# Kernel optimization log

Hardware: AMD Instinct MI355X
Metric: run time of the kernel (lower is better)

## Reference

```python
import jax, jax.numpy as jnp
import numpy as np

N, E, D = 10000, 640000, 128
H1, H2, OUT = 256, 256, 64
EPS = 1e-5

def _layernorm(h, g, b):
    m = jnp.mean(h, axis=-1, keepdims=True)
    v = jnp.mean((h - m) ** 2, axis=-1, keepdims=True)
    return (h - m) * jax.lax.rsqrt(v + EPS) * g + b

def setup_inputs() -> dict:
    key = jax.random.key(0)
    ks = jax.random.split(key, 20)
    def lin(k, fan_in, fan_out):
        bound = 1.0 / np.sqrt(fan_in)
        kw, kb = jax.random.split(k)
        W = jax.random.uniform(kw, (fan_in, fan_out), jnp.float32, -bound, bound)
        b = jax.random.uniform(kb, (fan_out,), jnp.float32, -bound, bound)
        return W, b
    pool_w, pool_b = lin(ks[0], D, D)
    w1, b1 = lin(ks[1], D, H1)
    w2, b2 = lin(ks[2], H1, H2)
    mu_w, mu_b = lin(ks[3], H2, OUT)
    lv_w, lv_b = lin(ks[4], H2, OUT)
    return {
        "x": jax.random.normal(ks[5], (N, D), jnp.float32),
        "edge_index": jax.random.randint(ks[6], (2, E), 0, N, jnp.int32),
        "edge_strength": jax.random.uniform(ks[7], (E,), jnp.float32),
        "ewmc": jnp.float32(0.5),
        "pool_w": pool_w, "pool_b": pool_b,
        "lnp_g": jnp.ones((D,), jnp.float32), "lnp_b": jnp.zeros((D,), jnp.float32),
        "w1": w1, "b1": b1,
        "ln1_g": jnp.ones((H1,), jnp.float32), "ln1_b": jnp.zeros((H1,), jnp.float32),
        "w2": w2, "b2": b2,
        "ln2_g": jnp.ones((H2,), jnp.float32), "ln2_b": jnp.zeros((H2,), jnp.float32),
        "mu_w": mu_w, "mu_b": mu_b,
        "lv_w": lv_w, "lv_b": lv_b,
    }

def reference(x, edge_index, edge_strength, ewmc, pool_w, pool_b, lnp_g, lnp_b,
              w1, b1, ln1_g, ln1_b, w2, b2, ln2_g, ln2_b, mu_w, mu_b, lv_w, lv_b):
    src, dst = edge_index[0], edge_index[1]
    coef = jax.nn.softplus(ewmc)
    # [E, D] gather + edge scaling
    msgs = x[src] * (1.0 + coef * edge_strength[:, None])
    pooled = jax.nn.relu(_layernorm(msgs @ pool_w + pool_b, lnp_g, lnp_b))
    # segment max by dst; torch_scatter fills empty segments with 0 and pooled >= 0
    agg = jax.ops.segment_max(pooled, dst, num_segments=x.shape[0])
    agg = jnp.maximum(agg, 0.0)
    h = jax.nn.relu(_layernorm(agg @ w1 + b1, ln1_g, ln1_b))
    h = jax.nn.relu(_layernorm(h @ w2 + b2, ln2_g, ln2_b))
    mu = h @ mu_w + mu_b
    logvar = h @ lv_w + lv_b
    std = jnp.exp(0.5 * logvar)
    return (mu, std)
```

## Files before the change

kernel.cpp:

```cpp
#include <hip/hip_runtime.h>
#include <math.h>

#define D_DIM   128
#define H1_DIM  256
#define H2_DIM  256
#define OUT_DIM 64
#define LN_EPS  1e-5f
#define NSHARD  4

typedef __attribute__((ext_vector_type(8))) short bf16x8;
typedef __attribute__((ext_vector_type(4))) float f32x4;

__device__ __forceinline__ unsigned short bf16rne(float v) {
    unsigned int b = __float_as_uint(v);
    return (unsigned short)((b + 0x7FFFu + ((b >> 16) & 1u)) >> 16);
}

union BFPack { unsigned int u[4]; bf16x8 v; };

__global__ __launch_bounds__(512) void k_pool(
        const float* __restrict__ x, const float* __restrict__ pw,
        const float* __restrict__ pb,
        unsigned short* __restrict__ y, float4* __restrict__ stat4,
        const int* __restrict__ ei, int* __restrict__ cnt, int E, int epb,
        const float* __restrict__ w1, const float* __restrict__ w2,
        const float* __restrict__ muw, const float* __restrict__ lvw,
        short* __restrict__ wp1, short* __restrict__ wp2,
        short* __restrict__ wpH) {
    __shared__ __align__(16) short aPack[4 * 64 * 8];
    __shared__ unsigned short yLds[16][128];
    __shared__ float sPart[16][8][3];
    const int tid  = threadIdx.x;
    const int w    = tid >> 6;
    const int lane = tid & 63;
    const int gq   = lane >> 4;
    const int c16  = lane & 15;
    const int row0 = blockIdx.x * 16;

    bf16x8 bfrag[4];
    {
        const int col = w * 16 + c16;
        const int kbase = gq * 8;
#pragma unroll
        for (int kt = 0; kt < 4; ++kt) {
            int k0 = kt * 32 + kbase;
            BFPack t;
#pragma unroll
            for (int jj = 0; jj < 4; ++jj) {
                float a = pw[(k0 + 2 * jj) * D_DIM + col];
                float b = pw[(k0 + 2 * jj + 1) * D_DIM + col];
                t.u[jj] = (unsigned int)bf16rne(a) | ((unsigned int)bf16rne(b) << 16);
            }
            bfrag[kt] = t.v;
        }
    }
    {
        int ebeg = blockIdx.x * epb;
        int eend = ebeg + epb; if (eend > E) eend = E;
        for (int e = ebeg + tid; e < eend; e += 512)
            atomicAdd(&cnt[ei[E + e] * NSHARD + (e & (NSHARD - 1))], 1);
    }
    {
        int r  = tid >> 5;
        int k0 = (tid & 31) * 4;
        float4 v = *(const float4*)&x[(size_t)(row0 + r) * D_DIM + k0];
        int kt = k0 >> 5, sub = (k0 >> 3) & 3, j = k0 & 7;
        int lp = r | (sub << 4);
        unsigned int u0 = (unsigned int)bf16rne(v.x) | ((unsigned int)bf16rne(v.y) << 16);
        unsigned int u1 = (unsigned int)bf16rne(v.z) | ((unsigned int)bf16rne(v.w) << 16);
        *(uint2*)&aPack[kt * 512 + lp * 8 + j] = make_uint2(u0, u1);
    }
    __syncthreads();

    f32x4 A = {0.f, 0.f, 0.f, 0.f};
#pragma unroll
    for (int kt = 0; kt < 4; ++kt) {
        bf16x8 av = *(bf16x8*)&aPack[(kt * 64 + lane) * 8];
        A = __builtin_amdgcn_mfma_f32_16x16x32_bf16(av, bfrag[kt], A, 0, 0, 0);
    }

    {
        float pbf = pb[w * 16 + c16];
#pragma unroll
        for (int r = 0; r < 4; ++r) {
            unsigned short h = bf16rne(A[r]);
            yLds[gq * 4 + r][w * 16 + c16] = h;
            float hf = __uint_as_float((unsigned int)h << 16);
            float s1 = hf, s2 = hf * hf, s3 = hf * pbf;
#pragma unroll
            for (int m = 1; m < 16; m <<= 1) {
                s1 += __shfl_xor(s1, m, 64);
                s2 += __shfl_xor(s2, m, 64);
                s3 += __shfl_xor(s3, m, 64);
            }
            if (c16 == 0) {
                sPart[gq * 4 + r][w][0] = s1;
                sPart[gq * 4 + r][w][1] = s2;
                sPart[gq * 4 + r][w][2] = s3;
            }
        }
    }
    __syncthreads();
    {
        int idx = tid * 4;
        int r = idx >> 7, c = idx & 127;
        *(uint2*)&y[(size_t)(row0 + r) * D_DIM + c] = *(const uint2*)&yLds[r][c];
    }
    if (tid < 16) {
        float t1 = 0.f, t2 = 0.f, t3 = 0.f;
#pragma unroll
        for (int ww = 0; ww < 8; ++ww) {
            t1 += sPart[tid][ww][0]; t2 += sPart[tid][ww][1]; t3 += sPart[tid][ww][2];
        }
        stat4[row0 + tid] = make_float4(t1 * (1.f / 128.f), t2 * (1.f / 128.f),
                                        t3 * (1.f / 128.f), 0.f);
    }
    if (blockIdx.x < 32) {
        int i = blockIdx.x * 512 + tid;
        const float* W; int Ndim, kt, ln, col; short* dst;
        if (i < 4096) {
            int q = i >> 6; ln = i & 63; kt = q & 3; int ct = q >> 2;
            W = w1; Ndim = H1_DIM; col = ct * 16 + (ln & 15); dst = wp1 + i * 8;
        } else if (i < 12288) {
            int i2 = i - 4096; int q = i2 >> 6; ln = i2 & 63; kt = q & 7; int ct = q >> 3;
            W = w2; Ndim = H2_DIM; col = ct * 16 + (ln & 15); dst = wp2 + i2 * 8;
        } else {
            int i3 = i - 12288; int q = i3 >> 6; ln = i3 & 63; kt = q & 7; int ct = q >> 3;
            Ndim = OUT_DIM; dst = wpH + i3 * 8;
            if (ct < 4) { W = muw; col = ct * 16 + (ln & 15); }
            else        { W = lvw; col = (ct - 4) * 16 + (ln & 15); }
        }
        int k0 = kt * 32 + (ln >> 4) * 8;
        unsigned int u[4];
#pragma unroll
        for (int jj = 0; jj < 4; ++jj) {
            float a = W[(k0 + 2 * jj) * Ndim + col];
            float b = W[(k0 + 2 * jj + 1) * Ndim + col];
            u[jj] = (unsigned int)bf16rne(a) | ((unsigned int)bf16rne(b) << 16);
        }
        *(uint4*)dst = make_uint4(u[0], u[1], u[2], u[3]);
    }
}

__global__ __launch_bounds__(1024) void k_scanA(
        const int* __restrict__ cnt, int* __restrict__ offs,
        int* __restrict__ bsum, int N4) {
    __shared__ int part[1024];
    const int t = threadIdx.x;
    const int idx = blockIdx.x * 1024 + t;
    int v = (idx < N4) ? cnt[idx] : 0;
    part[t] = v;
    __syncthreads();
    for (int off = 1; off < 1024; off <<= 1) {
        int n = (t >= off) ? part[t - off] : 0;
        __syncthreads();
        part[t] += n;
        __syncthreads();
    }
    if (idx < N4) offs[idx] = part[t] - v;
    if (t == 1023) bsum[blockIdx.x] = part[t];
}

__global__ __launch_bounds__(64) void k_scanB(
        const int* __restrict__ bsum, int* __restrict__ bbase,
        int* __restrict__ offs, float* __restrict__ consts,
        const float* __restrict__ ewmc, const float* __restrict__ pb,
        int nblk, int N4) {
    const int l = threadIdx.x;
    {
        float v0 = pb[l], v1 = pb[l + 64];
        float s1 = v0 + v1, s2 = v0 * v0 + v1 * v1;
#pragma unroll
        for (int off = 1; off < 64; off <<= 1) {
            s1 += __shfl_xor(s1, off, 64);
            s2 += __shfl_xor(s2, off, 64);
        }
        if (l == 0) {
            float xw = ewmc[0];
            consts[0] = (xw > 30.f) ? xw : log1pf(expf(xw));
            consts[1] = s1 * (1.f / 128.f);
            consts[2] = s2 * (1.f / 128.f);
        }
    }
    int val = (l < nblk) ? bsum[l] : 0;
    int orig = val;
#pragma unroll
    for (int off = 1; off < 64; off <<= 1) {
        int n = __shfl_up(val, off, 64);
        if (l >= off) val += n;
    }
    if (l < nblk) bbase[l] = val - orig;
    if (l == nblk - 1) offs[N4] = val;
}

__global__ __launch_bounds__(1024) void k_scanC(
        int* __restrict__ offs, int* __restrict__ head,
        const int* __restrict__ bbase, int N4) {
    int idx = blockIdx.x * 1024 + threadIdx.x;
    if (idx < N4) {
        int o = offs[idx] + bbase[blockIdx.x];
        offs[idx] = o;
        head[idx] = o;
    }
}

__global__ __launch_bounds__(256) void k_scatter(
        const int* __restrict__ ei, const float* __restrict__ es,
        const float* __restrict__ consts, const float4* __restrict__ stat4,
        int* __restrict__ head, float4* __restrict__ pairs, int E) {
    const float coef = consts[0], mpb = consts[1], mpb2 = consts[2];
    const int tid = threadIdx.x;
    const int e0 = blockIdx.x * 1024 + tid;
    int srcv[4], dstv[4]; float sv[4]; float4 st[4]; int pos[4]; bool ok[4];
#pragma unroll
    for (int u = 0; u < 4; ++u) {
        int e = e0 + u * 256;
        ok[u] = (e < E);
        if (ok[u]) { srcv[u] = ei[e]; dstv[u] = ei[E + e]; sv[u] = es[e]; }
    }
#pragma unroll
    for (int u = 0; u < 4; ++u) if (ok[u]) st[u] = stat4[srcv[u]];
#pragma unroll
    for (int u = 0; u < 4; ++u) if (ok[u]) {
        int e = e0 + u * 256;
        pos[u] = atomicAdd(&head[dstv[u] * NSHARD + (e & (NSHARD - 1))], 1);
    }
#pragma unroll
    for (int u = 0; u < 4; ++u) if (ok[u]) {
        float s = fmaf(coef, sv[u], 1.0f);
        float m   = fmaf(s, st[u].x, mpb);
        float et2 = fmaf(s * s, st[u].y, fmaf(2.f * s, st[u].z, mpb2));
        float inv = rsqrtf(et2 - m * m + LN_EPS);
        pairs[pos[u]] = make_float4(__int_as_float(srcv[u]), s, m, inv);
    }
}

#define GPROC(P, YB)                                                          \
    {                                                                         \
        float s = (P).y, m = (P).z, inv = (P).w;                              \
        float y0 = __uint_as_float((YB).x << 16);                             \
        float y1 = __uint_as_float((YB).x & 0xFFFF0000u);                     \
        float y2 = __uint_as_float((YB).y << 16);                             \
        float y3 = __uint_as_float((YB).y & 0xFFFF0000u);                     \
        float y4 = __uint_as_float((YB).z << 16);                             \
        float y5 = __uint_as_float((YB).z & 0xFFFF0000u);                     \
        float y6 = __uint_as_float((YB).w << 16);                             \
        float y7 = __uint_as_float((YB).w & 0xFFFF0000u);                     \
        mxA.x = fmaxf(mxA.x, fmaf(fmaf(s, y0, pbA.x) - m, inv * gA.x, bA.x)); \
        mxA.y = fmaxf(mxA.y, fmaf(fmaf(s, y1, pbA.y) - m, inv * gA.y, bA.y)); \
        mxA.z = fmaxf(mxA.z, fmaf(fmaf(s, y2, pbA.z) - m, inv * gA.z, bA.z)); \
        mxA.w = fmaxf(mxA.w, fmaf(fmaf(s, y3, pbA.w) - m, inv * gA.w, bA.w)); \
        mxB.x = fmaxf(mxB.x, fmaf(fmaf(s, y4, pbB.x) - m, inv * gB.x, bB.x)); \
        mxB.y = fmaxf(mxB.y, fmaf(fmaf(s, y5, pbB.y) - m, inv * gB.y, bB.y)); \
        mxB.z = fmaxf(mxB.z, fmaf(fmaf(s, y6, pbB.z) - m, inv * gB.z, bB.z)); \
        mxB.w = fmaxf(mxB.w, fmaf(fmaf(s, y7, pbB.w) - m, inv * gB.w, bB.w)); \
    }

__global__ __launch_bounds__(256) void k_gather(
        const float4* __restrict__ pairs, const int* __restrict__ offs,
        const unsigned short* __restrict__ y, const float* __restrict__ pb,
        const float* __restrict__ g, const float* __restrict__ b,
        float* __restrict__ agg, int N) {
    const int node = blockIdx.x * 4 + (threadIdx.x >> 6);
    if (node >= N) return;
    const int lane = threadIdx.x & 63;
    const int sub  = lane >> 4;
    const int q    = lane & 15;
    const int d0   = q * 8;
    const float4 pbA = *(const float4*)&pb[d0], pbB = *(const float4*)&pb[d0 + 4];
    const float4 gA  = *(const float4*)&g[d0],  gB  = *(const float4*)&g[d0 + 4];
    const float4 bA  = *(const float4*)&b[d0],  bB  = *(const float4*)&b[d0 + 4];
    float4 mxA = make_float4(-INFINITY, -INFINITY, -INFINITY, -INFINITY);
    float4 mxB = mxA;
    int j = offs[node * NSHARD];
    const int end = offs[node * NSHARD + NSHARD];
    for (; j + 12 <= end; j += 12) {
        float4 p[3]; uint4 yb[3];
#pragma unroll
        for (int u = 0; u < 3; ++u) p[u] = pairs[j + 4 * u + sub];
#pragma unroll
        for (int u = 0; u < 3; ++u)
            yb[u] = *(const uint4*)&y[(size_t)__float_as_int(p[u].x) * D_DIM + d0];
#pragma unroll
        for (int u = 0; u < 3; ++u) GPROC(p[u], yb[u]);
    }
    for (; j + 4 <= end; j += 4) {
        float4 p = pairs[j + sub];
        uint4 yb = *(const uint4*)&y[(size_t)__float_as_int(p.x) * D_DIM + d0];
        GPROC(p, yb);
    }
    if (j < end) {
        int rem = end - j;
        float4 p = pairs[j + (sub < rem ? sub : 0)];
        uint4 yb = *(const uint4*)&y[(size_t)__float_as_int(p.x) * D_DIM + d0];
        GPROC(p, yb);
    }
    mxA.x = fmaxf(mxA.x, __shfl_xor(mxA.x, 16, 64));
    mxA.y = fmaxf(mxA.y, __shfl_xor(mxA.y, 16, 64));
    mxA.z = fmaxf(mxA.z, __shfl_xor(mxA.z, 16, 64));
    mxA.w = fmaxf(mxA.w, __shfl_xor(mxA.w, 16, 64));
    mxB.x = fmaxf(mxB.x, __shfl_xor(mxB.x, 16, 64));
    mxB.y = fmaxf(mxB.y, __shfl_xor(mxB.y, 16, 64));
    mxB.z = fmaxf(mxB.z, __shfl_xor(mxB.z, 16, 64));
    mxB.w = fmaxf(mxB.w, __shfl_xor(mxB.w, 16, 64));
    mxA.x = fmaxf(mxA.x, __shfl_xor(mxA.x, 32, 64));
    mxA.y = fmaxf(mxA.y, __shfl_xor(mxA.y, 32, 64));
    mxA.z = fmaxf(mxA.z, __shfl_xor(mxA.z, 32, 64));
    mxA.w = fmaxf(mxA.w, __shfl_xor(mxA.w, 32, 64));
    mxB.x = fmaxf(mxB.x, __shfl_xor(mxB.x, 32, 64));
    mxB.y = fmaxf(mxB.y, __shfl_xor(mxB.y, 32, 64));
    mxB.z = fmaxf(mxB.z, __shfl_xor(mxB.z, 32, 64));
    mxB.w = fmaxf(mxB.w, __shfl_xor(mxB.w, 32, 64));
    if (sub == 0) {
        float4 oA, oB;
        oA.x = fmaxf(mxA.x, 0.f); oA.y = fmaxf(mxA.y, 0.f);
        oA.z = fmaxf(mxA.z, 0.f); oA.w = fmaxf(mxA.w, 0.f);
        oB.x = fmaxf(mxB.x, 0.f); oB.y = fmaxf(mxB.y, 0.f);
        oB.z = fmaxf(mxB.z, 0.f); oB.w = fmaxf(mxB.w, 0.f);
        *(float4*)&agg[(size_t)node * D_DIM + d0]     = oA;
        *(float4*)&agg[(size_t)node * D_DIM + d0 + 4] = oB;
    }
}

__global__ __launch_bounds__(512) void k_mlp(
        const float* __restrict__ agg,
        const short* __restrict__ wp1, const short* __restrict__ wp2,
        const short* __restrict__ wpH,
        const float* __restrict__ b1, const float* __restrict__ g1,
        const float* __restrict__ bb1,
        const float* __restrict__ b2, const float* __restrict__ g2,
        const float* __restrict__ bb2,
        const float* __restrict__ mub, const float* __restrict__ lvb,
        float* __restrict__ out, int N) {
    __shared__ __align__(16) short aPack[8 * 64 * 8];
    __shared__ float sPart[16][8][2];
    __shared__ float sM[16], sI[16];
    const int tid  = threadIdx.x;
    const int w    = tid >> 6;
    const int lane = tid & 63;
    const int gq   = lane >> 4;
    const int c16  = lane & 15;
    const int row0 = blockIdx.x * 16;

    {
        int r  = tid >> 5;
        int k0 = (tid & 31) * 4;
        float4 v = *(const float4*)&agg[(size_t)(row0 + r) * D_DIM + k0];
        int kt = k0 >> 5, sub = (k0 >> 3) & 3, j = k0 & 7;
        int lp = r | (sub << 4);
        unsigned int u0 = (unsigned int)bf16rne(v.x) | ((unsigned int)bf16rne(v.y) << 16);
        unsigned int u1 = (unsigned int)bf16rne(v.z) | ((unsigned int)bf16rne(v.w) << 16);
        *(uint2*)&aPack[kt * 512 + lp * 8 + j] = make_uint2(u0, u1);
    }
    __syncthreads();

    const int ct0 = 2 * w, ct1 = 2 * w + 1;
    f32x4 A0 = {0.f, 0.f, 0.f, 0.f}, A1 = {0.f, 0.f, 0.f, 0.f};

#pragma unroll
    for (int kt = 0; kt < 4; ++kt) {
        bf16x8 av = *(bf16x8*)&aPack[(kt * 64 + lane) * 8];
        bf16x8 bv0 = *(const bf16x8*)&wp1[((ct0 * 4 + kt) * 64 + lane) * 8];
        bf16x8 bv1 = *(const bf16x8*)&wp1[((ct1 * 4 + kt) * 64 + lane) * 8];
        A0 = __builtin_amdgcn_mfma_f32_16x16x32_bf16(av, bv0, A0, 0, 0, 0);
        A1 = __builtin_amdgcn_mfma_f32_16x16x32_bf16(av, bv1, A1, 0, 0, 0);
    }
    {
        int col0 = ct0 * 16 + c16, col1 = ct1 * 16 + c16;
        float bias0 = b1[col0], bias1 = b1[col1];
        float v0[4], v1[4];
#pragma unroll
        for (int r = 0; r < 4; ++r) {
            v0[r] = A0[r] + bias0; v1[r] = A1[r] + bias1;
            float s1 = v0[r] + v1[r];
            float s2 = v0[r] * v0[r] + v1[r] * v1[r];
#pragma unroll
            for (int m = 1; m < 16; m <<= 1) {
                s1 += __shfl_xor(s1, m, 64);
                s2 += __shfl_xor(s2, m, 64);
            }
            if (c16 == 0) { sPart[gq * 4 + r][w][0] = s1; sPart[gq * 4 + r][w][1] = s2; }
        }
        __syncthreads();
        if (tid < 16) {
            float t1 = 0.f, t2 = 0.f;
#pragma unroll
            for (int ww = 0; ww < 8; ++ww) { t1 += sPart[tid][ww][0]; t2 += sPart[tid][ww][1]; }
            float m = t1 * (1.f / 256.f);
            sM[tid] = m;
            sI[tid] = rsqrtf(t2 * (1.f / 256.f) - m * m + LN_EPS);
        }
        __syncthreads();
        float gc0 = g1[col0], bc0 = bb1[col0];
        float gc1 = g1[col1], bc1 = bb1[col1];
#pragma unroll
        for (int r = 0; r < 4; ++r) {
            int row = gq * 4 + r;
            float m = sM[row], inv = sI[row];
            float h0 = fmaxf(fmaf((v0[r] - m) * inv, gc0, bc0), 0.f);
            float h1 = fmaxf(fmaf((v1[r] - m) * inv, gc1, bc1), 0.f);
            aPack[(col0 >> 5) * 512 + (row | (((col0 >> 3) & 3) << 4)) * 8 + (col0 & 7)] = (short)bf16rne(h0);
            aPack[(col1 >> 5) * 512 + (row | (((col1 >> 3) & 3) << 4)) * 8 + (col1 & 7)] = (short)bf16rne(h1);
        }
    }
    __syncthreads();

    A0 = (f32x4){0.f, 0.f, 0.f, 0.f}; A1 = (f32x4){0.f, 0.f, 0.f, 0.f};
#pragma unroll
    for (int kt = 0; kt < 8; ++kt) {
        bf16x8 av = *(bf16x8*)&aPack[(kt * 64 + lane) * 8];
        bf16x8 bv0 = *(const bf16x8*)&wp2[((ct0 * 8 + kt) * 64 + lane) * 8];
        bf16x8 bv1 = *(const bf16x8*)&wp2[((ct1 * 8 + kt) * 64 + lane) * 8];
        A0 = __builtin_amdgcn_mfma_f32_16x16x32_bf16(av, bv0, A0, 0, 0, 0);
        A1 = __builtin_amdgcn_mfma_f32_16x16x32_bf16(av, bv1, A1, 0, 0, 0);
    }
    {
        int col0 = ct0 * 16 + c16, col1 = ct1 * 16 + c16;
        float bias0 = b2[col0], bias1 = b2[col1];
        float v0[4], v1[4];
#pragma unroll
        for (int r = 0; r < 4; ++r) {
            v0[r] = A0[r] + bias0; v1[r] = A1[r] + bias1;
            float s1 = v0[r] + v1[r];
            float s2 = v0[r] * v0[r] + v1[r] * v1[r];
#pragma unroll
            for (int m = 1; m < 16; m <<= 1) {
                s1 += __shfl_xor(s1, m, 64);
                s2 += __shfl_xor(s2, m, 64);
            }
            if (c16 == 0) { sPart[gq * 4 + r][w][0] = s1; sPart[gq * 4 + r][w][1] = s2; }
        }
        __syncthreads();
        if (tid < 16) {
            float t1 = 0.f, t2 = 0.f;
#pragma unroll
            for (int ww = 0; ww < 8; ++ww) { t1 += sPart[tid][ww][0]; t2 += sPart[tid][ww][1]; }
            float m = t1 * (1.f / 256.f);
            sM[tid] = m;
            sI[tid] = rsqrtf(t2 * (1.f / 256.f) - m * m + LN_EPS);
        }
        __syncthreads();
        float gc0 = g2[col0], bc0 = bb2[col0];
        float gc1 = g2[col1], bc1 = bb2[col1];
#pragma unroll
        for (int r = 0; r < 4; ++r) {
            int row = gq * 4 + r;
            float m = sM[row], inv = sI[row];
            float h0 = fmaxf(fmaf((v0[r] - m) * inv, gc0, bc0), 0.f);
            float h1 = fmaxf(fmaf((v1[r] - m) * inv, gc1, bc1), 0.f);
            aPack[(col0 >> 5) * 512 + (row | (((col0 >> 3) & 3) << 4)) * 8 + (col0 & 7)] = (short)bf16rne(h0);
            aPack[(col1 >> 5) * 512 + (row | (((col1 >> 3) & 3) << 4)) * 8 + (col1 & 7)] = (short)bf16rne(h1);
        }
    }
    __syncthreads();

    {
        f32x4 H = {0.f, 0.f, 0.f, 0.f};
#pragma unroll
        for (int kt = 0; kt < 8; ++kt) {
            bf16x8 av = *(bf16x8*)&aPack[(kt * 64 + lane) * 8];
            bf16x8 bv = *(const bf16x8*)&wpH[((w * 8 + kt) * 64 + lane) * 8];
            H = __builtin_amdgcn_mfma_f32_16x16x32_bf16(av, bv, H, 0, 0, 0);
        }
        int colh = (w & 3) * 16 + c16;
        if (w < 4) {
            float bias = mub[colh];
#pragma unroll
            for (int r = 0; r < 4; ++r)
                out[(size_t)(row0 + gq * 4 + r) * OUT_DIM + colh] = H[r] + bias;
        } else {
            float bias = lvb[colh];
#pragma unroll
            for (int r = 0; r < 4; ++r)
                out[(size_t)N * OUT_DIM + (size_t)(row0 + gq * 4 + r) * OUT_DIM + colh] =
                    expf(0.5f * (H[r] + bias));
        }
    }
}

extern "C" void kernel_launch(void* const* d_in, const int* in_sizes, int n_in,
                              void* d_out, int out_size, void* d_ws, size_t ws_size,
                              hipStream_t stream) {
    const float* x      = (const float*)d_in[0];
    const int*   ei     = (const int*)  d_in[1];
    const float* es     = (const float*)d_in[2];
    const float* ewmc   = (const float*)d_in[3];
    const float* pool_w = (const float*)d_in[4];
    const float* pool_b = (const float*)d_in[5];
    const float* lnp_g  = (const float*)d_in[6];
    const float* lnp_b  = (const float*)d_in[7];
    const float* w1     = (const float*)d_in[8];
    const float* b1     = (const float*)d_in[9];
    const float* ln1_g  = (const float*)d_in[10];
    const float* ln1_b  = (const float*)d_in[11];
    const float* w2     = (const float*)d_in[12];
    const float* b2     = (const float*)d_in[13];
    const float* ln2_g  = (const float*)d_in[14];
    const float* ln2_b  = (const float*)d_in[15];
    const float* mu_w   = (const float*)d_in[16];
    const float* mu_b   = (const float*)d_in[17];
    const float* lv_w   = (const float*)d_in[18];
    const float* lv_b   = (const float*)d_in[19];

    const int N  = in_sizes[0] / D_DIM;
    const int E  = in_sizes[2];
    const int N4 = N * NSHARD;
    const int nblkScan = (N4 + 1023) / 1024;

    float*  ws     = (float*)d_ws;
    float*  consts = ws;
    float4* stat4  = (float4*)(ws + 16);
    unsigned short* y = (unsigned short*)(ws + 16 + 4 * (size_t)N);
    float*  agg    = ws + 16 + 4 * (size_t)N + (size_t)N * D_DIM / 2;
    size_t  w      = 16 + 4 * (size_t)N + (size_t)N * D_DIM / 2 + (size_t)N * D_DIM;
    int*    cnt    = (int*)(ws + w); w += N4;
    int*    offs   = (int*)(ws + w); w += N4 + 1;
    int*    head   = (int*)(ws + w); w += N4;
    int*    bsum   = (int*)(ws + w); w += 64;
    int*    bbase  = (int*)(ws + w); w += 64;
    w = (w + 3) & ~(size_t)3;
    short*  wp1    = (short*)(ws + w); w += 16384;
    short*  wp2    = (short*)(ws + w); w += 32768;
    short*  wpH    = (short*)(ws + w); w += 16384;
    float4* pairs  = (float4*)(ws + w);

    const int nbPool = N / 16;
    const int epb    = (E + nbPool - 1) / nbPool;

    hipMemsetAsync(cnt, 0, (size_t)N4 * sizeof(int), stream);
    k_pool<<<nbPool, 512, 0, stream>>>(x, pool_w, pool_b, y, stat4, ei, cnt, E,
                                       epb, w1, w2, mu_w, lv_w, wp1, wp2, wpH);
    k_scanA<<<nblkScan, 1024, 0, stream>>>(cnt, offs, bsum, N4);
    k_scanB<<<1, 64, 0, stream>>>(bsum, bbase, offs, consts, ewmc, pool_b,
                                  nblkScan, N4);
    k_scanC<<<nblkScan, 1024, 0, stream>>>(offs, head, bbase, N4);
    k_scatter<<<(E + 1023) / 1024, 256, 0, stream>>>(ei, es, consts, stat4,
                                                     head, pairs, E);
    k_gather<<<(N + 3) / 4, 256, 0, stream>>>(pairs, offs, y,
                                              pool_b, lnp_g, lnp_b, agg, N);
    k_mlp<<<N / 16, 512, 0, stream>>>(agg, wp1, wp2, wpH,
                                      b1, ln1_g, ln1_b,
                                      b2, ln2_g, ln2_b,
                                      mu_b, lv_b, (float*)d_out, N);
}
```

Baseline: 118.5 us.

## Fuse segment-max gather into MLP kernel and widen scatter per-thread work

Merges the gather/segment-max kernel into the MLP kernel. Each of the 8 waves in a 512-thread block aggregates two of the block's 16 nodes and writes bf16 results straight into the shared-memory A-pack, so the fp32 agg buffer is never written to or read from global memory. Separately, the scatter kernel now handles 8 edges per thread instead of 4, halving its grid size. The fusion saves a kernel launch and the agg round trip, but gives the MLP blocks a serial, load-imbalanced gather phase with fewer nodes in flight per wave, which may hide gather latency less well.

```diff
diff --git a/kernel.cpp b/kernel.cpp
--- a/kernel.cpp
+++ b/kernel.cpp
@@ -210,23 +210,23 @@
         int* __restrict__ head, float4* __restrict__ pairs, int E) {
     const float coef = consts[0], mpb = consts[1], mpb2 = consts[2];
     const int tid = threadIdx.x;
-    const int e0 = blockIdx.x * 1024 + tid;
-    int srcv[4], dstv[4]; float sv[4]; float4 st[4]; int pos[4]; bool ok[4];
-#pragma unroll
-    for (int u = 0; u < 4; ++u) {
+    const int e0 = blockIdx.x * 2048 + tid;
+    int srcv[8], dstv[8]; float sv[8]; float4 st[8]; int pos[8]; bool ok[8];
+#pragma unroll
+    for (int u = 0; u < 8; ++u) {
         int e = e0 + u * 256;
         ok[u] = (e < E);
         if (ok[u]) { srcv[u] = ei[e]; dstv[u] = ei[E + e]; sv[u] = es[e]; }
     }
 #pragma unroll
-    for (int u = 0; u < 4; ++u) if (ok[u]) st[u] = stat4[srcv[u]];
-#pragma unroll
-    for (int u = 0; u < 4; ++u) if (ok[u]) {
+    for (int u = 0; u < 8; ++u) if (ok[u]) st[u] = stat4[srcv[u]];
+#pragma unroll
+    for (int u = 0; u < 8; ++u) if (ok[u]) {
         int e = e0 + u * 256;
         pos[u] = atomicAdd(&head[dstv[u] * NSHARD + (e & (NSHARD - 1))], 1);
     }
 #pragma unroll
-    for (int u = 0; u < 4; ++u) if (ok[u]) {
+    for (int u = 0; u < 8; ++u) if (ok[u]) {
         float s = fmaf(coef, sv[u], 1.0f);
         float m   = fmaf(s, st[u].x, mpb);
         float et2 = fmaf(s * s, st[u].y, fmaf(2.f * s, st[u].z, mpb2));
@@ -256,74 +256,10 @@
         mxB.w = fmaxf(mxB.w, fmaf(fmaf(s, y7, pbB.w) - m, inv * gB.w, bB.w)); \
     }
 
-__global__ __launch_bounds__(256) void k_gather(
+__global__ __launch_bounds__(512) void k_gmlp(
         const float4* __restrict__ pairs, const int* __restrict__ offs,
         const unsigned short* __restrict__ y, const float* __restrict__ pb,
         const float* __restrict__ g, const float* __restrict__ b,
-        float* __restrict__ agg, int N) {
-    const int node = blockIdx.x * 4 + (threadIdx.x >> 6);
-    if (node >= N) return;
-    const int lane = threadIdx.x & 63;
-    const int sub  = lane >> 4;
-    const int q    = lane & 15;
-    const int d0   = q * 8;
-    const float4 pbA = *(const float4*)&pb[d0], pbB = *(const float4*)&pb[d0 + 4];
-    const float4 gA  = *(const float4*)&g[d0],  gB  = *(const float4*)&g[d0 + 4];
-    const float4 bA  = *(const float4*)&b[d0],  bB  = *(const float4*)&b[d0 + 4];
-    float4 mxA = make_float4(-INFINITY, -INFINITY, -INFINITY, -INFINITY);
-    float4 mxB = mxA;
-    int j = offs[node * NSHARD];
-    const int end = offs[node * NSHARD + NSHARD];
-    for (; j + 12 <= end; j += 12) {
-        float4 p[3]; uint4 yb[3];
-#pragma unroll
-        for (int u = 0; u < 3; ++u) p[u] = pairs[j + 4 * u + sub];
-#pragma unroll
-        for (int u = 0; u < 3; ++u)
-            yb[u] = *(const uint4*)&y[(size_t)__float_as_int(p[u].x) * D_DIM + d0];
-#pragma unroll
-        for (int u = 0; u < 3; ++u) GPROC(p[u], yb[u]);
-    }
-    for (; j + 4 <= end; j += 4) {
-        float4 p = pairs[j + sub];
-        uint4 yb = *(const uint4*)&y[(size_t)__float_as_int(p.x) * D_DIM + d0];
-        GPROC(p, yb);
-    }
-    if (j < end) {
-        int rem = end - j;
-        float4 p = pairs[j + (sub < rem ? sub : 0)];
-        uint4 yb = *(const uint4*)&y[(size_t)__float_as_int(p.x) * D_DIM + d0];
-        GPROC(p, yb);
-    }
-    mxA.x = fmaxf(mxA.x, __shfl_xor(mxA.x, 16, 64));
-    mxA.y = fmaxf(mxA.y, __shfl_xor(mxA.y, 16, 64));
-    mxA.z = fmaxf(mxA.z, __shfl_xor(mxA.z, 16, 64));
-    mxA.w = fmaxf(mxA.w, __shfl_xor(mxA.w, 16, 64));
-    mxB.x = fmaxf(mxB.x, __shfl_xor(mxB.x, 16, 64));
-    mxB.y = fmaxf(mxB.y, __shfl_xor(mxB.y, 16, 64));
-    mxB.z = fmaxf(mxB.z, __shfl_xor(mxB.z, 16, 64));
-    mxB.w = fmaxf(mxB.w, __shfl_xor(mxB.w, 16, 64));
-    mxA.x = fmaxf(mxA.x, __shfl_xor(mxA.x, 32, 64));
-    mxA.y = fmaxf(mxA.y, __shfl_xor(mxA.y, 32, 64));
-    mxA.z = fmaxf(mxA.z, __shfl_xor(mxA.z, 32, 64));
-    mxA.w = fmaxf(mxA.w, __shfl_xor(mxA.w, 32, 64));
-    mxB.x = fmaxf(mxB.x, __shfl_xor(mxB.x, 32, 64));
-    mxB.y = fmaxf(mxB.y, __shfl_xor(mxB.y, 32, 64));
-    mxB.z = fmaxf(mxB.z, __shfl_xor(mxB.z, 32, 64));
-    mxB.w = fmaxf(mxB.w, __shfl_xor(mxB.w, 32, 64));
-    if (sub == 0) {
-        float4 oA, oB;
-        oA.x = fmaxf(mxA.x, 0.f); oA.y = fmaxf(mxA.y, 0.f);
-        oA.z = fmaxf(mxA.z, 0.f); oA.w = fmaxf(mxA.w, 0.f);
-        oB.x = fmaxf(mxB.x, 0.f); oB.y = fmaxf(mxB.y, 0.f);
-        oB.z = fmaxf(mxB.z, 0.f); oB.w = fmaxf(mxB.w, 0.f);
-        *(float4*)&agg[(size_t)node * D_DIM + d0]     = oA;
-        *(float4*)&agg[(size_t)node * D_DIM + d0 + 4] = oB;
-    }
-}
-
-__global__ __launch_bounds__(512) void k_mlp(
-        const float* __restrict__ agg,
         const short* __restrict__ wp1, const short* __restrict__ wp2,
         const short* __restrict__ wpH,
         const float* __restrict__ b1, const float* __restrict__ g1,
@@ -343,14 +279,70 @@
     const int row0 = blockIdx.x * 16;
 
     {
-        int r  = tid >> 5;
-        int k0 = (tid & 31) * 4;
-        float4 v = *(const float4*)&agg[(size_t)(row0 + r) * D_DIM + k0];
-        int kt = k0 >> 5, sub = (k0 >> 3) & 3, j = k0 & 7;
-        int lp = r | (sub << 4);
-        unsigned int u0 = (unsigned int)bf16rne(v.x) | ((unsigned int)bf16rne(v.y) << 16);
-        unsigned int u1 = (unsigned int)bf16rne(v.z) | ((unsigned int)bf16rne(v.w) << 16);
-        *(uint2*)&aPack[kt * 512 + lp * 8 + j] = make_uint2(u0, u1);
+        const int sub = lane >> 4;
+        const int q   = lane & 15;
+        const int d0  = q * 8;
+        const float4 pbA = *(const float4*)&pb[d0], pbB = *(const float4*)&pb[d0 + 4];
+        const float4 gA  = *(const float4*)&g[d0],  gB  = *(const float4*)&g[d0 + 4];
+        const float4 bA  = *(const float4*)&b[d0],  bB  = *(const float4*)&b[d0 + 4];
+#pragma unroll
+        for (int nn = 0; nn < 2; ++nn) {
+            const int r = 2 * w + nn;
+            const int node = row0 + r;
+            float4 mxA = make_float4(-INFINITY, -INFINITY, -INFINITY, -INFINITY);
+            float4 mxB = mxA;
+            int j = offs[node * NSHARD];
+            const int end = offs[node * NSHARD + NSHARD];
+            for (; j + 12 <= end; j += 12) {
+                float4 p[3]; uint4 yb[3];
+#pragma unroll
+                for (int u = 0; u < 3; ++u) p[u] = pairs[j + 4 * u + sub];
+#pragma unroll
+                for (int u = 0; u < 3; ++u)
+                    yb[u] = *(const uint4*)&y[(size_t)__float_as_int(p[u].x) * D_DIM + d0];
+#pragma unroll
+                for (int u = 0; u < 3; ++u) GPROC(p[u], yb[u]);
+            }
+            for (; j + 4 <= end; j += 4) {
+                float4 p = pairs[j + sub];
+                uint4 yb = *(const uint4*)&y[(size_t)__float_as_int(p.x) * D_DIM + d0];
+                GPROC(p, yb);
+            }
+            if (j < end) {
+                int rem = end - j;
+                float4 p = pairs[j + (sub < rem ? sub : 0)];
+                uint4 yb = *(const uint4*)&y[(size_t)__float_as_int(p.x) * D_DIM + d0];
+                GPROC(p, yb);
+            }
+            mxA.x = fmaxf(mxA.x, __shfl_xor(mxA.x, 16, 64));
+            mxA.y = fmaxf(mxA.y, __shfl_xor(mxA.y, 16, 64));
+            mxA.z = fmaxf(mxA.z, __shfl_xor(mxA.z, 16, 64));
+            mxA.w = fmaxf(mxA.w, __shfl_xor(mxA.w, 16, 64));
+            mxB.x = fmaxf(mxB.x, __shfl_xor(mxB.x, 16, 64));
+            mxB.y = fmaxf(mxB.y, __shfl_xor(mxB.y, 16, 64));
+            mxB.z = fmaxf(mxB.z, __shfl_xor(mxB.z, 16, 64));
+            mxB.w = fmaxf(mxB.w, __shfl_xor(mxB.w, 16, 64));
+            mxA.x = fmaxf(mxA.x, __shfl_xor(mxA.x, 32, 64));
+            mxA.y = fmaxf(mxA.y, __shfl_xor(mxA.y, 32, 64));
+            mxA.z = fmaxf(mxA.z, __shfl_xor(mxA.z, 32, 64));
+            mxA.w = fmaxf(mxA.w, __shfl_xor(mxA.w, 32, 64));
+            mxB.x = fmaxf(mxB.x, __shfl_xor(mxB.x, 32, 64));
+            mxB.y = fmaxf(mxB.y, __shfl_xor(mxB.y, 32, 64));
+            mxB.z = fmaxf(mxB.z, __shfl_xor(mxB.z, 32, 64));
+            mxB.w = fmaxf(mxB.w, __shfl_xor(mxB.w, 32, 64));
+            if (sub == 0) {
+                unsigned int u0 = (unsigned int)bf16rne(fmaxf(mxA.x, 0.f))
+                                | ((unsigned int)bf16rne(fmaxf(mxA.y, 0.f)) << 16);
+                unsigned int u1 = (unsigned int)bf16rne(fmaxf(mxA.z, 0.f))
+                                | ((unsigned int)bf16rne(fmaxf(mxA.w, 0.f)) << 16);
+                unsigned int u2 = (unsigned int)bf16rne(fmaxf(mxB.x, 0.f))
+                                | ((unsigned int)bf16rne(fmaxf(mxB.y, 0.f)) << 16);
+                unsigned int u3 = (unsigned int)bf16rne(fmaxf(mxB.z, 0.f))
+                                | ((unsigned int)bf16rne(fmaxf(mxB.w, 0.f)) << 16);
+                int kt = q >> 2, sfr = q & 3, lp = r | (sfr << 4);
+                *(uint4*)&aPack[kt * 512 + lp * 8] = make_uint4(u0, u1, u2, u3);
+            }
+        }
     }
     __syncthreads();
 
@@ -511,8 +503,7 @@
     float*  consts = ws;
     float4* stat4  = (float4*)(ws + 16);
     unsigned short* y = (unsigned short*)(ws + 16 + 4 * (size_t)N);
-    float*  agg    = ws + 16 + 4 * (size_t)N + (size_t)N * D_DIM / 2;
-    size_t  w      = 16 + 4 * (size_t)N + (size_t)N * D_DIM / 2 + (size_t)N * D_DIM;
+    size_t  w      = 16 + 4 * (size_t)N + (size_t)N * D_DIM / 2;
     int*    cnt    = (int*)(ws + w); w += N4;
     int*    offs   = (int*)(ws + w); w += N4 + 1;
     int*    head   = (int*)(ws + w); w += N4;
@@ -534,12 +525,11 @@
     k_scanB<<<1, 64, 0, stream>>>(bsum, bbase, offs, consts, ewmc, pool_b,
                                   nblkScan, N4);
     k_scanC<<<nblkScan, 1024, 0, stream>>>(offs, head, bbase, N4);
-    k_scatter<<<(E + 1023) / 1024, 256, 0, stream>>>(ei, es, consts, stat4,
+    k_scatter<<<(E + 2047) / 2048, 256, 0, stream>>>(ei, es, consts, stat4,
                                                      head, pairs, E);
-    k_gather<<<(N + 3) / 4, 256, 0, stream>>>(pairs, offs, y,
-                                              pool_b, lnp_g, lnp_b, agg, N);
-    k_mlp<<<N / 16, 512, 0, stream>>>(agg, wp1, wp2, wpH,
-                                      b1, ln1_g, ln1_b,
-                                      b2, ln2_g, ln2_b,
-                                      mu_b, lv_b, (float*)d_out, N);
-}
+    k_gmlp<<<N / 16, 512, 0, stream>>>(pairs, offs, y, pool_b, lnp_g, lnp_b,
+                                       wp1, wp2, wpH,
+                                       b1, ln1_g, ln1_b,
+                                       b2, ln2_g, ln2_b,
+                                       mu_b, lv_b, (float*)d_out, N);
+}
```

New measurement: 128.6 us. +8.6%, slower.
